# Kernel tuning notes

Measured on AMD Instinct MI355X. Metric: run time of the kernel, lower is better.

The kernel has to match this reference:

```python
import jax, jax.numpy as jnp
import numpy as np

MAX_LEVEL = 4
CURV = 1.0
MAX_NORM = 0.95
N_ITER = 10


def project_to_poincare(x):
    # Rescale points whose norm exceeds max_norm / sqrt(c) back onto the ball.
    norm = jnp.linalg.norm(x, axis=-1, keepdims=True)
    max_r = MAX_NORM / jnp.sqrt(jnp.asarray(CURV, x.dtype))
    return jnp.where(norm > max_r, x / (norm + 1e-12) * max_r, x)


def poincare_distance(x, y):
    # d(x,y) = arccosh(1 + 2c||x-y||^2 / ((1-c||x||^2)(1-c||y||^2))) / sqrt(c)
    sq = jnp.sum((x - y) ** 2, axis=-1)
    nx = jnp.sum(x * x, axis=-1)
    ny = jnp.sum(y * y, axis=-1)
    denom = jnp.maximum((1.0 - CURV * nx) * (1.0 - CURV * ny), 1e-12)
    arg = 1.0 + 2.0 * CURV * sq / denom
    return jnp.arccosh(jnp.maximum(arg, 1.0 + 1e-7)) / jnp.sqrt(CURV)


def setup_inputs() -> dict:
    key = jax.random.key(0)
    k1, k2 = jax.random.split(key)
    B, D = 1048576, 32
    z = jax.random.normal(k1, (B, D), dtype=jnp.float32)
    batch_indices = jax.random.randint(k2, (B,), 0, 19683, dtype=jnp.int64)
    level_weights = jnp.array([0.5 ** i for i in range(MAX_LEVEL)], dtype=jnp.float32)
    return {"z": z, "batch_indices": batch_indices, "level_weights": level_weights}


def reference(z, batch_indices, level_weights):
    z_hyp = project_to_poincare(z)
    B = z.shape[0]
    ones = jnp.ones((B,), dtype=z.dtype)
    total_loss = jnp.asarray(0.0, dtype=z.dtype)
    for level in range(1, MAX_LEVEL + 1):
        n_seg = 3 ** level
        seg = (batch_indices // (3 ** (9 - level))).astype(jnp.int32)
        counts = jax.ops.segment_sum(ones, seg, num_segments=n_seg)          # [n_seg]
        sums = jax.ops.segment_sum(z_hyp, seg, num_segments=n_seg)           # [n_seg, D]
        safe_counts = jnp.maximum(counts, 1.0)[:, None]
        euc_mean = sums / safe_counts                                        # weighted (uniform) mean
        # Frechet-mean iteration: direction = sum_i w_i (x_i - mean) = euc_mean - mean
        mean = project_to_poincare(euc_mean)
        for _ in range(N_ITER):
            mean = project_to_poincare(mean + 0.1 * (euc_mean - mean))
        cent = mean[seg]                                                     # [B, D]
        dists = poincare_distance(z_hyp, cent)                               # [B]
        dist_mean = jax.ops.segment_sum(dists, seg, num_segments=n_seg) / jnp.maximum(counts, 1.0)
        valid = counts >= 2.0                                                # clusters with <2 pts skipped
        level_loss = jnp.sum(jnp.where(valid, dist_mean, 0.0))
        n_unique = jnp.sum(counts > 0.0)
        total_loss = total_loss + level_weights[level - 1] * level_loss / jnp.maximum(n_unique, 1.0)
    return total_loss
```

## Files before the change

### kernel.cpp

```cpp
#include <hip/hip_runtime.h>
#include <math.h>


#define MAXR  0.95f
#define MAXR2 0.9025f
#define LN2F  0.6931471805599453f

#define NPART 768
#define PPG   96
#define HCOLS 2673
#define OFF_HSUM8 (1024 * HCOLS)
#define OFF_DSUM  (OFF_HSUM8 + 8 * HCOLS)
#define OFF_CENT  (OFF_DSUM + 8 * 324)
#define OFF_CNT   (OFF_CENT + 120 * 32)
#define OFF_CN4   (OFF_CNT + 120)
#define OFF_TI4   (OFF_CN4 + 324)

__device__ __forceinline__ float fsqrt(float x) { return __builtin_amdgcn_sqrtf(x); }
__device__ __forceinline__ float frcp(float x)  { return __builtin_amdgcn_rcpf(x); }
__device__ __forceinline__ float frsq(float x)  { return __builtin_amdgcn_rsqf(x); }

__device__ __forceinline__ float red8_dpp(float v) {
    v += __int_as_float(__builtin_amdgcn_update_dpp(0, __float_as_int(v), 0xB1, 0xF, 0xF, 1));
    v += __int_as_float(__builtin_amdgcn_update_dpp(0, __float_as_int(v), 0x4E, 0xF, 0xF, 1));
    v += __int_as_float(__builtin_amdgcn_update_dpp(0, __float_as_int(v), 0x141, 0xF, 0xF, 1));
    return v;
}

__device__ __forceinline__ float red32_dpp(float v) {
    v += __int_as_float(__builtin_amdgcn_update_dpp(0, __float_as_int(v), 0xB1, 0xF, 0xF, 1));
    v += __int_as_float(__builtin_amdgcn_update_dpp(0, __float_as_int(v), 0x4E, 0xF, 0xF, 1));
    v += __int_as_float(__builtin_amdgcn_update_dpp(0, __float_as_int(v), 0x141, 0xF, 0xF, 1));
    v += __int_as_float(__builtin_amdgcn_update_dpp(0, __float_as_int(v), 0x140, 0xF, 0xF, 1));
    v += __shfl_xor(v, 16, 32);
    return v;
}

__device__ __forceinline__ int dup_rank(int s4, int g, int sub) {
    int sj = __shfl(s4, sub * 8, 64);
    unsigned long long eq = __ballot(sj == s4);
    unsigned int row = (unsigned int)(eq >> (g * 8));
    return __popc(row & ((1u << g) - 1u));
}

__global__ __launch_bounds__(256) void pass1_hist(
        const float* __restrict__ z, const int* __restrict__ idx,
        float* __restrict__ part, int B) {
    __shared__ float lsum[4][81][36];
    const int tid = threadIdx.x;
    for (int j = tid; j < 4 * 81 * 36; j += 256) (&lsum[0][0][0])[j] = 0.f;
    __syncthreads();

    const int w = tid >> 6;
    const int g = (tid & 63) >> 3;
    const int sub = tid & 7;
    const int STRIDE = gridDim.x * 256;
    const int base0 = blockIdx.x * 256 + w * 64 + g;
    const int nfull = B / STRIDE;
    float* const lw = &lsum[w][0][0];

    for (int it = 0; it < nfull; ++it) {
        const int ib = it * STRIDE + base0;
        float4 xv[8];
        int s4v[8], rank[8];
#pragma unroll
        for (int b = 0; b < 8; ++b)
            xv[b] = *(const float4*)(z + (size_t)(ib + b * 8) * 32 + sub * 4);
#pragma unroll
        for (int b = 0; b < 8; ++b)
            s4v[b] = idx[ib + b * 8] / 243;
#pragma unroll
        for (int b = 0; b < 8; ++b) {
            const float nx = red8_dpp(xv[b].x * xv[b].x + xv[b].y * xv[b].y +
                                      xv[b].z * xv[b].z + xv[b].w * xv[b].w);
            const float s = (nx > MAXR2) ? MAXR * frsq(nx) : 1.0f;
            xv[b].x *= s; xv[b].y *= s; xv[b].z *= s; xv[b].w *= s;
        }
#pragma unroll
        for (int b = 0; b < 8; ++b)
            rank[b] = dup_rank(s4v[b], g, sub);
#pragma unroll
        for (int b = 0; b < 8; ++b) {
            float* row = lw + s4v[b] * 36;
            for (int r = 0;; ++r) {
                if (!__any(rank[b] == r)) break;
                if (rank[b] == r) {
                    float4 cur = *(float4*)(row + sub * 4);
                    cur.x += xv[b].x; cur.y += xv[b].y;
                    cur.z += xv[b].z; cur.w += xv[b].w;
                    *(float4*)(row + sub * 4) = cur;
                    if (sub == 0) row[32] += 1.0f;
                }
            }
        }
    }
    if (B % STRIDE) {
        const int ib = nfull * STRIDE + base0;
        for (int b = 0; b < 8; ++b) {
            const int i = ib + b * 8;
            const bool act = i < B;
            float4 x = act ? *(const float4*)(z + (size_t)i * 32 + sub * 4)
                           : make_float4(0.f, 0.f, 0.f, 0.f);
            int s4 = act ? idx[i] / 243 : 81 + g;
            const float nx = red8_dpp(x.x * x.x + x.y * x.y + x.z * x.z + x.w * x.w);
            const float s = (nx > MAXR2) ? MAXR * frsq(nx) : 1.0f;
            x.x *= s; x.y *= s; x.z *= s; x.w *= s;
            int rank = dup_rank(s4, g, sub);
            for (int r = 0;; ++r) {
                if (!__any(rank == r)) break;
                if (act && rank == r) {
                    float* row = lw + s4 * 36;
                    float4 cur = *(float4*)(row + sub * 4);
                    cur.x += x.x; cur.y += x.y; cur.z += x.z; cur.w += x.w;
                    *(float4*)(row + sub * 4) = cur;
                    if (sub == 0) row[32] += 1.0f;
                }
            }
        }
    }
    __syncthreads();
    float* myslice = part + (size_t)blockIdx.x * HCOLS;
    for (int j = tid; j < HCOLS; j += 256) {
        const int r = j / 33, c = j - r * 33;
        myslice[j] = lsum[0][r][c] + lsum[1][r][c] +
                     lsum[2][r][c] + lsum[3][r][c];
    }
}

__global__ __launch_bounds__(256) void pass2a_reduce(
        const float* __restrict__ part, float* __restrict__ hsum8,
        float* __restrict__ dsum) {
    const int tid = threadIdx.x;
    const int group = blockIdx.x / 11;
    const int jb = blockIdx.x - group * 11;
    const int j = jb * 256 + tid;
    if (blockIdx.x == 0)
        for (int k = tid; k < 8 * 324; k += 256) dsum[k] = 0.f;
    if (j < HCOLS) {
        const float* p0 = part + (size_t)(group * PPG) * HCOLS + j;
        float s0 = 0.f, s1 = 0.f, s2 = 0.f, s3 = 0.f;
        for (int b = 0; b < PPG; b += 4) {
            s0 += p0[(size_t)b * HCOLS];
            s1 += p0[(size_t)(b + 1) * HCOLS];
            s2 += p0[(size_t)(b + 2) * HCOLS];
            s3 += p0[(size_t)(b + 3) * HCOLS];
        }
        hsum8[group * HCOLS + j] = (s0 + s1) + (s2 + s3);
    }
}

__global__ __launch_bounds__(256) void pass2_centroids(
        const float* __restrict__ hsum8,
        float* __restrict__ cent, float* __restrict__ cnt_all,
        float* __restrict__ cnorm4, int* __restrict__ tidx4) {
    __shared__ float euc[120][33];
    __shared__ float cn[120];
    const int tid = threadIdx.x;
    for (int j = tid; j < HCOLS; j += 256) {
        float s = 0.f;
#pragma unroll
        for (int p = 0; p < 8; ++p) s += hsum8[p * HCOLS + j];
        const int r = j / 33, c = j - r * 33;
        euc[39 + r][c] = s;
    }
    __syncthreads();
    for (int j = tid; j < 27 * 33; j += 256) {
        const int r = j / 33, c = j - r * 33;
        euc[12 + r][c] = euc[39 + 3 * r][c] + euc[40 + 3 * r][c] + euc[41 + 3 * r][c];
    }
    __syncthreads();
    for (int j = tid; j < 9 * 33; j += 256) {
        const int r = j / 33, c = j - r * 33;
        euc[3 + r][c] = euc[12 + 3 * r][c] + euc[13 + 3 * r][c] + euc[14 + 3 * r][c];
    }
    __syncthreads();
    for (int j = tid; j < 3 * 33; j += 256) {
        const int r = j / 33, c = j - r * 33;
        euc[r][c] = euc[3 + 3 * r][c] + euc[4 + 3 * r][c] + euc[5 + 3 * r][c];
    }
    __syncthreads();
    const int lane = tid & 31;
    const int grp = tid >> 5;
    for (int t = grp; t < 120; t += 8) {
        const float sum = euc[t][lane];
        const float cnt = euc[t][32];
        const float em = sum / fmaxf(cnt, 1.0f);
        float m = em;
        {
            float norm = sqrtf(red32_dpp(m * m));
            if (norm > MAXR) m *= MAXR / (norm + 1e-12f);
        }
        for (int it = 0; it < 10; ++it) {
            float v = m + 0.1f * (em - m);
            float norm = sqrtf(red32_dpp(v * v));
            if (norm > MAXR) v *= MAXR / (norm + 1e-12f);
            m = v;
        }
        cent[t * 32 + lane] = m;
        float ny = red32_dpp(m * m);
        if (lane == 0) { cnt_all[t] = cnt; cn[t] = 1.0f - ny; }
    }
    __syncthreads();
    if (tid < 81) {
        const int s4 = tid;
        const int d3 = s4 / 3, d9 = d3 / 3, d27 = d9 / 3;
        const int t0 = d27, t1 = 3 + d9, t2 = 12 + d3, t3 = 39 + s4;
        ((int4*)tidx4)[s4] = make_int4(t0, t1, t2, t3);
        ((float4*)cnorm4)[s4] = make_float4(cn[t0], cn[t1], cn[t2], cn[t3]);
    }
}

__global__ __launch_bounds__(256) void pass3_dist(
        const float* __restrict__ z, const int* __restrict__ idx,
        const float* __restrict__ cent, const float* __restrict__ cnorm4,
        const int* __restrict__ tidx4, float* __restrict__ dsum, int B) {
    __shared__ float lcent[120 * 32];
    __shared__ float4 lcn4[81];
    __shared__ int4 ltl4[81];
    __shared__ float ld[4][81][4];
    const int tid = threadIdx.x;
    for (int j = tid; j < 120 * 32; j += 256) lcent[j] = cent[j];
    for (int j = tid; j < 324; j += 256) ((float*)lcn4)[j] = cnorm4[j];
    for (int j = tid; j < 324; j += 256) ((int*)ltl4)[j] = tidx4[j];
    for (int j = tid; j < 4 * 81 * 4; j += 256) (&ld[0][0][0])[j] = 0.f;
    __syncthreads();

    const int w = tid >> 6;
    const int g = (tid & 63) >> 3;
    const int sub = tid & 7;
    const int STRIDE = gridDim.x * 128;
    const int base0 = blockIdx.x * 128 + w * 32 + g;
    const int nfull = B / STRIDE;

    for (int it = 0; it < nfull; ++it) {
        const int ib = it * STRIDE + base0;
        float4 xv[4];
        int s4v[4], rank[4];
        float dl[4][4];
#pragma unroll
        for (int b = 0; b < 4; ++b)
            xv[b] = *(const float4*)(z + (size_t)(ib + b * 8) * 32 + sub * 4);
#pragma unroll
        for (int b = 0; b < 4; ++b)
            s4v[b] = idx[ib + b * 8] / 243;
#pragma unroll
        for (int b = 0; b < 4; ++b) {
            float nx = red8_dpp(xv[b].x * xv[b].x + xv[b].y * xv[b].y +
                                xv[b].z * xv[b].z + xv[b].w * xv[b].w);
            const float s = (nx > MAXR2) ? MAXR * frsq(nx) : 1.0f;
            xv[b].x *= s; xv[b].y *= s; xv[b].z *= s; xv[b].w *= s;
            nx = nx * s * s;
            const float ah = 0.5f * (1.0f - nx);
            const float c2a = 1.0f + nx;
            const int s4 = s4v[b];
            const int4 t4 = ltl4[s4];
            const float4 cn4 = lcn4[s4];
            const int tls[4] = {t4.x, t4.y, t4.z, t4.w};
            const float bnys[4] = {cn4.x, cn4.y, cn4.z, cn4.w};
#pragma unroll
            for (int l = 0; l < 4; ++l) {
                const int t = tls[l];
                const float4 c = *(const float4*)(lcent + t * 32 + sub * 4);
                const float dot = red8_dpp(xv[b].x * c.x + xv[b].y * c.y +
                                           xv[b].z * c.z + xv[b].w * c.w);
                const float bny = bnys[l];
                const float sq = fmaf(-2.0f, dot, c2a - bny);
                const float d = fmaxf(ah * bny, 5e-13f);
                float tt = sq * frcp(d);
                tt = fmaxf(tt, 1e-7f);
                dl[b][l] = __log2f(1.0f + tt + fsqrt(tt * (tt + 2.0f)));
            }
        }
#pragma unroll
        for (int b = 0; b < 4; ++b)
            rank[b] = dup_rank(s4v[b], g, sub);
#pragma unroll
        for (int b = 0; b < 4; ++b) {
            float* row = &ld[w][s4v[b]][0];
            for (int r = 0;; ++r) {
                if (!__any(rank[b] == r)) break;
                if (rank[b] == r && sub == 0) {
                    float4 cur = *(float4*)row;
                    cur.x += dl[b][0]; cur.y += dl[b][1];
                    cur.z += dl[b][2]; cur.w += dl[b][3];
                    *(float4*)row = cur;
                }
            }
        }
    }
    if (B % STRIDE) {
        const int ib = nfull * STRIDE + base0;
        for (int b = 0; b < 4; ++b) {
            const int i = ib + b * 8;
            const bool act = i < B;
            float4 x = act ? *(const float4*)(z + (size_t)i * 32 + sub * 4)
                           : make_float4(0.f, 0.f, 0.f, 0.f);
            const int s4 = act ? idx[i] / 243 : 0;
            float nx = red8_dpp(x.x * x.x + x.y * x.y + x.z * x.z + x.w * x.w);
            const float s = (nx > MAXR2) ? MAXR * frsq(nx) : 1.0f;
            x.x *= s; x.y *= s; x.z *= s; x.w *= s;
            nx = nx * s * s;
            const float ah = 0.5f * (1.0f - nx);
            const float c2a = 1.0f + nx;
            const int4 t4 = ltl4[s4];
            const float4 cn4 = lcn4[s4];
            const int tls[4] = {t4.x, t4.y, t4.z, t4.w};
            const float bnys[4] = {cn4.x, cn4.y, cn4.z, cn4.w};
            float dl[4];
#pragma unroll
            for (int l = 0; l < 4; ++l) {
                const int t = tls[l];
                const float4 c = *(const float4*)(lcent + t * 32 + sub * 4);
                const float dot = red8_dpp(x.x * c.x + x.y * c.y +
                                           x.z * c.z + x.w * c.w);
                const float bny = bnys[l];
                const float sq = fmaf(-2.0f, dot, c2a - bny);
                const float d = fmaxf(ah * bny, 5e-13f);
                float tt = sq * frcp(d);
                tt = fmaxf(tt, 1e-7f);
                dl[l] = __log2f(1.0f + tt + fsqrt(tt * (tt + 2.0f)));
            }
            int rank = dup_rank(act ? s4 : -1 - g, g, sub);
            for (int r = 0;; ++r) {
                if (!__any(rank == r)) break;
                if (act && rank == r && sub == 0) {
                    float* row = &ld[w][s4][0];
                    float4 cur = *(float4*)row;
                    cur.x += dl[0]; cur.y += dl[1]; cur.z += dl[2]; cur.w += dl[3];
                    *(float4*)row = cur;
                }
            }
        }
    }
    __syncthreads();
    float* dpart = dsum + (blockIdx.x & 7) * 324;
    for (int j = tid; j < 81 * 4; j += 256) {
        const float v = (&ld[0][0][0])[j] + (&ld[1][0][0])[j] +
                        (&ld[2][0][0])[j] + (&ld[3][0][0])[j];
        unsafeAtomicAdd(&dpart[j], v);
    }
}

__global__ __launch_bounds__(128) void pass4_final(
        const float* __restrict__ dsum, const float* __restrict__ cnt_all,
        const float* __restrict__ w, float* __restrict__ out) {
    __shared__ float sl[81];
    __shared__ float su[81];
    const int tid = threadIdx.x;
    const int toff[4] = {0, 3, 12, 39};
    const int nsegs[4] = {3, 9, 27, 81};
    float total = 0.f;
    for (int l = 0; l < 4; ++l) {
        const int n_seg = nsegs[l];
        const int ch = 81 / n_seg;
        __syncthreads();
        if (tid < n_seg) {
            float cnt = cnt_all[toff[l] + tid];
            float ds = 0.f;
            for (int p = 0; p < 8; ++p)
                for (int k = 0; k < ch; ++k)
                    ds += dsum[p * 324 + (tid * ch + k) * 4 + l];
            sl[tid] = (cnt >= 2.0f) ? ds * LN2F / fmaxf(cnt, 1.0f) : 0.f;
            su[tid] = (cnt > 0.0f) ? 1.f : 0.f;
        }
        __syncthreads();
        if (tid == 0) {
            float ll = 0.f, nu = 0.f;
            for (int s = 0; s < n_seg; ++s) { ll += sl[s]; nu += su[s]; }
            total += w[l] * ll / fmaxf(nu, 1.0f);
        }
    }
    if (tid == 0) out[0] = total;
}

extern "C" void kernel_launch(void* const* d_in, const int* in_sizes, int n_in,
                              void* d_out, int out_size, void* d_ws, size_t ws_size,
                              hipStream_t stream) {
    const float* z   = (const float*)d_in[0];
    const int*   idx = (const int*)d_in[1];
    const float* w   = (const float*)d_in[2];
    float* out = (float*)d_out;
    float* ws  = (float*)d_ws;
    const int B = in_sizes[1];

    float* part    = ws;
    float* hsum8   = ws + OFF_HSUM8;
    float* dsum    = ws + OFF_DSUM;
    float* cent    = ws + OFF_CENT;
    float* cnt_all = ws + OFF_CNT;
    float* cnorm4  = ws + OFF_CN4;
    int*   tidx4   = (int*)(ws + OFF_TI4);

    pass1_hist<<<NPART, 256, 0, stream>>>(z, idx, part, B);
    pass2a_reduce<<<88, 256, 0, stream>>>(part, hsum8, dsum);
    pass2_centroids<<<1, 256, 0, stream>>>(hsum8, cent, cnt_all, cnorm4, tidx4);
    pass3_dist<<<1792, 256, 0, stream>>>(z, idx, cent, cnorm4, tidx4, dsum, B);
    pass4_final<<<1, 128, 0, stream>>>(dsum, cnt_all, w, out);
}
```

Before: 113.9 us.

## Spread per-level acosh math across sub-lanes and double rows per iteration

Each 8-lane group now computes the four centroid dot products once, then lanes 0-3 each evaluate the distance/log for one hierarchy level. Before, every lane redundantly computed all four transcendental chains. Each lane writes its own level's scalar into the shared accumulator, replacing the float4 update from lane 0. The grid stride doubles so each wave handles 8 rows per iteration, which adds more loads in flight but also more registers for the 8 buffered float4s.

```diff
diff --git a/kernel.cpp b/kernel.cpp
--- a/kernel.cpp
+++ b/kernel.cpp
@@ -215,12 +215,12 @@
         const float* __restrict__ cent, const float* __restrict__ cnorm4,
         const int* __restrict__ tidx4, float* __restrict__ dsum, int B) {
     __shared__ float lcent[120 * 32];
-    __shared__ float4 lcn4[81];
+    __shared__ float lcn[81 * 4];
     __shared__ int4 ltl4[81];
     __shared__ float ld[4][81][4];
     const int tid = threadIdx.x;
     for (int j = tid; j < 120 * 32; j += 256) lcent[j] = cent[j];
-    for (int j = tid; j < 324; j += 256) ((float*)lcn4)[j] = cnorm4[j];
+    for (int j = tid; j < 324; j += 256) lcn[j] = cnorm4[j];
     for (int j = tid; j < 324; j += 256) ((int*)ltl4)[j] = tidx4[j];
     for (int j = tid; j < 4 * 81 * 4; j += 256) (&ld[0][0][0])[j] = 0.f;
     __syncthreads();
@@ -228,69 +228,63 @@
     const int w = tid >> 6;
     const int g = (tid & 63) >> 3;
     const int sub = tid & 7;
-    const int STRIDE = gridDim.x * 128;
-    const int base0 = blockIdx.x * 128 + w * 32 + g;
+    const int lvl = sub & 3;
+    const bool sb1 = (sub & 1) != 0;
+    const bool sb2 = (sub & 2) != 0;
+    const int STRIDE = gridDim.x * 256;
+    const int base0 = blockIdx.x * 256 + w * 64 + g;
     const int nfull = B / STRIDE;
 
     for (int it = 0; it < nfull; ++it) {
         const int ib = it * STRIDE + base0;
-        float4 xv[4];
-        int s4v[4], rank[4];
-        float dl[4][4];
-#pragma unroll
-        for (int b = 0; b < 4; ++b)
+        float4 xv[8];
+        int s4v[8];
+#pragma unroll
+        for (int b = 0; b < 8; ++b)
             xv[b] = *(const float4*)(z + (size_t)(ib + b * 8) * 32 + sub * 4);
 #pragma unroll
-        for (int b = 0; b < 4; ++b)
+        for (int b = 0; b < 8; ++b)
             s4v[b] = idx[ib + b * 8] / 243;
 #pragma unroll
-        for (int b = 0; b < 4; ++b) {
+        for (int b = 0; b < 8; ++b) {
             float nx = red8_dpp(xv[b].x * xv[b].x + xv[b].y * xv[b].y +
                                 xv[b].z * xv[b].z + xv[b].w * xv[b].w);
             const float s = (nx > MAXR2) ? MAXR * frsq(nx) : 1.0f;
-            xv[b].x *= s; xv[b].y *= s; xv[b].z *= s; xv[b].w *= s;
+            const float px = xv[b].x * s, py = xv[b].y * s,
+                        pz = xv[b].z * s, pw = xv[b].w * s;
             nx = nx * s * s;
             const float ah = 0.5f * (1.0f - nx);
             const float c2a = 1.0f + nx;
             const int s4 = s4v[b];
             const int4 t4 = ltl4[s4];
-            const float4 cn4 = lcn4[s4];
-            const int tls[4] = {t4.x, t4.y, t4.z, t4.w};
-            const float bnys[4] = {cn4.x, cn4.y, cn4.z, cn4.w};
-#pragma unroll
-            for (int l = 0; l < 4; ++l) {
-                const int t = tls[l];
-                const float4 c = *(const float4*)(lcent + t * 32 + sub * 4);
-                const float dot = red8_dpp(xv[b].x * c.x + xv[b].y * c.y +
-                                           xv[b].z * c.z + xv[b].w * c.w);
-                const float bny = bnys[l];
-                const float sq = fmaf(-2.0f, dot, c2a - bny);
-                const float d = fmaxf(ah * bny, 5e-13f);
-                float tt = sq * frcp(d);
-                tt = fmaxf(tt, 1e-7f);
-                dl[b][l] = __log2f(1.0f + tt + fsqrt(tt * (tt + 2.0f)));
-            }
-        }
-#pragma unroll
-        for (int b = 0; b < 4; ++b)
-            rank[b] = dup_rank(s4v[b], g, sub);
-#pragma unroll
-        for (int b = 0; b < 4; ++b) {
-            float* row = &ld[w][s4v[b]][0];
+            const float4 c0 = *(const float4*)(lcent + t4.x * 32 + sub * 4);
+            const float4 c1 = *(const float4*)(lcent + t4.y * 32 + sub * 4);
+            const float4 c2 = *(const float4*)(lcent + t4.z * 32 + sub * 4);
+            const float4 c3 = *(const float4*)(lcent + t4.w * 32 + sub * 4);
+            const float d0 = red8_dpp(px * c0.x + py * c0.y + pz * c0.z + pw * c0.w);
+            const float d1 = red8_dpp(px * c1.x + py * c1.y + pz * c1.z + pw * c1.w);
+            const float d2 = red8_dpp(px * c2.x + py * c2.y + pz * c2.z + pw * c2.w);
+            const float d3 = red8_dpp(px * c3.x + py * c3.y + pz * c3.z + pw * c3.w);
+            const float bny = lcn[(s4 << 2) | lvl];
+            const float ta = sb1 ? d1 : d0;
+            const float tb = sb1 ? d3 : d2;
+            const float dsel = sb2 ? tb : ta;
+            const float sq = fmaf(-2.0f, dsel, c2a - bny);
+            const float dd = fmaxf(ah * bny, 5e-13f);
+            float tt = sq * frcp(dd);
+            tt = fmaxf(tt, 1e-7f);
+            const float dlv = __log2f(1.0f + tt + fsqrt(tt * (tt + 2.0f)));
+            const int rank = dup_rank(s4, g, sub);
             for (int r = 0;; ++r) {
-                if (!__any(rank[b] == r)) break;
-                if (rank[b] == r && sub == 0) {
-                    float4 cur = *(float4*)row;
-                    cur.x += dl[b][0]; cur.y += dl[b][1];
-                    cur.z += dl[b][2]; cur.w += dl[b][3];
-                    *(float4*)row = cur;
-                }
+                if (!__any(rank == r)) break;
+                if (rank == r && sub < 4)
+                    ld[w][s4][lvl] += dlv;
             }
         }
     }
     if (B % STRIDE) {
         const int ib = nfull * STRIDE + base0;
-        for (int b = 0; b < 4; ++b) {
+        for (int b = 0; b < 8; ++b) {
             const int i = ib + b * 8;
             const bool act = i < B;
             float4 x = act ? *(const float4*)(z + (size_t)i * 32 + sub * 4)
@@ -298,37 +292,33 @@
             const int s4 = act ? idx[i] / 243 : 0;
             float nx = red8_dpp(x.x * x.x + x.y * x.y + x.z * x.z + x.w * x.w);
             const float s = (nx > MAXR2) ? MAXR * frsq(nx) : 1.0f;
-            x.x *= s; x.y *= s; x.z *= s; x.w *= s;
+            const float px = x.x * s, py = x.y * s, pz = x.z * s, pw = x.w * s;
             nx = nx * s * s;
             const float ah = 0.5f * (1.0f - nx);
             const float c2a = 1.0f + nx;
             const int4 t4 = ltl4[s4];
-            const float4 cn4 = lcn4[s4];
-            const int tls[4] = {t4.x, t4.y, t4.z, t4.w};
-            const float bnys[4] = {cn4.x, cn4.y, cn4.z, cn4.w};
-            float dl[4];
-#pragma unroll
-            for (int l = 0; l < 4; ++l) {
-                const int t = tls[l];
-                const float4 c = *(const float4*)(lcent + t * 32 + sub * 4);
-                const float dot = red8_dpp(x.x * c.x + x.y * c.y +
-                                           x.z * c.z + x.w * c.w);
-                const float bny = bnys[l];
-                const float sq = fmaf(-2.0f, dot, c2a - bny);
-                const float d = fmaxf(ah * bny, 5e-13f);
-                float tt = sq * frcp(d);
-                tt = fmaxf(tt, 1e-7f);
-                dl[l] = __log2f(1.0f + tt + fsqrt(tt * (tt + 2.0f)));
-            }
-            int rank = dup_rank(act ? s4 : -1 - g, g, sub);
+            const float4 c0 = *(const float4*)(lcent + t4.x * 32 + sub * 4);
+            const float4 c1 = *(const float4*)(lcent + t4.y * 32 + sub * 4);
+            const float4 c2 = *(const float4*)(lcent + t4.z * 32 + sub * 4);
+            const float4 c3 = *(const float4*)(lcent + t4.w * 32 + sub * 4);
+            const float d0 = red8_dpp(px * c0.x + py * c0.y + pz * c0.z + pw * c0.w);
+            const float d1 = red8_dpp(px * c1.x + py * c1.y + pz * c1.z + pw * c1.w);
+            const float d2 = red8_dpp(px * c2.x + py * c2.y + pz * c2.z + pw * c2.w);
+            const float d3 = red8_dpp(px * c3.x + py * c3.y + pz * c3.z + pw * c3.w);
+            const float bny = lcn[(s4 << 2) | lvl];
+            const float ta = sb1 ? d1 : d0;
+            const float tb = sb1 ? d3 : d2;
+            const float dsel = sb2 ? tb : ta;
+            const float sq = fmaf(-2.0f, dsel, c2a - bny);
+            const float dd = fmaxf(ah * bny, 5e-13f);
+            float tt = sq * frcp(dd);
+            tt = fmaxf(tt, 1e-7f);
+            const float dlv = __log2f(1.0f + tt + fsqrt(tt * (tt + 2.0f)));
+            const int rank = dup_rank(act ? s4 : -1 - g, g, sub);
             for (int r = 0;; ++r) {
                 if (!__any(rank == r)) break;
-                if (act && rank == r && sub == 0) {
-                    float* row = &ld[w][s4][0];
-                    float4 cur = *(float4*)row;
-                    cur.x += dl[0]; cur.y += dl[1]; cur.z += dl[2]; cur.w += dl[3];
-                    *(float4*)row = cur;
-                }
+                if (act && rank == r && sub < 4)
+                    ld[w][s4][lvl] += dlv;
             }
         }
     }
```

New measurement: 113.8 us. No clear change (-0.2%).
